# Kernel optimization log

Hardware: AMD Instinct MI355X
Metric: run time of the kernel (lower is better)

## Reference

```python
import jax, jax.numpy as jnp
import numpy as np

N = 100000       # nodes
E = 640000       # edges
G = 2048         # graphs in batch
IN_C, HID, NCLS = 3, 128, 4


def setup_inputs() -> dict:
    key = jax.random.key(0)
    ks = jax.random.split(key, 16)
    x = jax.random.normal(ks[0], (N, IN_C), dtype=jnp.float32)
    edge_index = jax.random.randint(ks[1], (2, E), 0, N, dtype=jnp.int64)
    batch = jnp.sort(jax.random.randint(ks[2], (N,), 0, G, dtype=jnp.int64))
    def glorot(k, shape):
        lim = np.sqrt(6.0 / (shape[0] + shape[1])).astype(np.float32)
        return jax.random.uniform(k, shape, jnp.float32, -lim, lim)
    return {
        "x": x, "edge_index": edge_index, "batch": batch,
        "W1": glorot(ks[3], (IN_C, HID)), "b1": jnp.zeros((HID,), jnp.float32),
        "W2": glorot(ks[4], (HID, HID)),  "b2": jnp.zeros((HID,), jnp.float32),
        "W3": glorot(ks[5], (HID, HID)),  "b3": jnp.zeros((HID,), jnp.float32),
        "W4": glorot(ks[6], (HID, HID)),  "b4": jnp.zeros((HID,), jnp.float32),
        "Wfc": glorot(ks[7], (HID, NCLS)), "bfc": jnp.zeros((NCLS,), jnp.float32),
    }


def _gcn_norm(edge_index):
    # Add self loops, then symmetric normalization D^{-1/2} (A+I) D^{-1/2}.
    loop = jnp.arange(N, dtype=edge_index.dtype)
    row = jnp.concatenate([edge_index[0], loop])  # source
    col = jnp.concatenate([edge_index[1], loop])  # target (aggregation side)
    deg = jax.ops.segment_sum(jnp.ones_like(col, dtype=jnp.float32), col,
                              num_segments=N)
    dinv = jnp.where(deg > 0, jax.lax.rsqrt(deg), 0.0)
    norm = dinv[row] * dinv[col]  # [E+N]
    return row, col, norm


def _gcn_layer(x, W, b, row, col, norm):
    h = x @ W                                 # [N, out]
    msg = h[row] * norm[:, None]              # gather + scale, [E+N, out]
    out = jax.ops.segment_sum(msg, col, num_segments=N)
    return out + b


def reference(x, edge_index, batch, W1, b1, W2, b2, W3, b3, W4, b4, Wfc, bfc):
    row, col, norm = _gcn_norm(edge_index)
    h = jax.nn.relu(_gcn_layer(x, W1, b1, row, col, norm))
    h = jax.nn.relu(_gcn_layer(h, W2, b2, row, col, norm))
    h = jax.nn.relu(_gcn_layer(h, W3, b3, row, col, norm))
    h = jax.nn.relu(_gcn_layer(h, W4, b4, row, col, norm))
    # global mean pool over graphs
    sums = jax.ops.segment_sum(h, batch, num_segments=G)           # [G, HID]
    cnt = jax.ops.segment_sum(jnp.ones((N,), jnp.float32), batch,
                              num_segments=G)
    pooled = sums / jnp.maximum(cnt, 1.0)[:, None]
    return pooled @ Wfc + bfc                                      # [G, NCLS]
```

## Files before the change

kernel.cpp:

```cpp
#include <hip/hip_runtime.h>
#include <hip/hip_bf16.h>

#define N_NODES  100000
#define N_EDGES  640000
#define N_GRAPHS 2048
#define HID      128
#define NB_SCAN  391
#define TILE     32
#define LDW      136

typedef _Float16 half_t;
typedef __attribute__((ext_vector_type(4))) _Float16 half4;
typedef __attribute__((ext_vector_type(8))) _Float16 half8;
typedef __attribute__((ext_vector_type(4))) float floatx4;

__global__ void k_prep(const int* __restrict__ col, int* __restrict__ deg,
                       const float* __restrict__ x, float4* __restrict__ xp,
                       const float* __restrict__ W2, const float* __restrict__ W3,
                       const float* __restrict__ W4, half_t* __restrict__ Wt) {
    int idx = blockIdx.x * 256 + threadIdx.x;
    if (idx < N_EDGES) atomicAdd(&deg[col[idx]], 1);
    if (idx < N_NODES) xp[idx] = make_float4(x[idx * 3 + 0], x[idx * 3 + 1], x[idx * 3 + 2], 0.f);
    if (idx < 3 * 128 * 128) {
        int l = idx >> 14;
        int e = idx & 16383;
        int cin = e >> 7, cout = e & 127;
        const float* W = (l == 0) ? W2 : ((l == 1) ? W3 : W4);
        Wt[l * 16384 + cout * 128 + cin] = (half_t)W[cin * 128 + cout];
    }
}

__global__ void k_scan1(const int* __restrict__ deg, int* __restrict__ row_ptr,
                        int* __restrict__ bsum, float* __restrict__ dinv) {
    __shared__ int s[256];
    int tid = threadIdx.x;
    int i = blockIdx.x * 256 + tid;
    int d = (i < N_NODES) ? deg[i] : 0;
    if (i < N_NODES) dinv[i] = rsqrtf((float)(d + 1));
    s[tid] = d;
    __syncthreads();
    for (int off = 1; off < 256; off <<= 1) {
        int v = (tid >= off) ? s[tid - off] : 0;
        __syncthreads();
        s[tid] += v;
        __syncthreads();
    }
    if (i < N_NODES) row_ptr[i] = s[tid] - d;
    if (tid == 255) bsum[blockIdx.x] = s[255];
}

__global__ void k_scan2(int* __restrict__ bsum) {
    __shared__ int s[512];
    int tid = threadIdx.x;
    int v = (tid < NB_SCAN) ? bsum[tid] : 0;
    s[tid] = v;
    __syncthreads();
    for (int off = 1; off < 512; off <<= 1) {
        int u = (tid >= off) ? s[tid - off] : 0;
        __syncthreads();
        s[tid] += u;
        __syncthreads();
    }
    if (tid < NB_SCAN) bsum[tid] = s[tid] - v;
}

__global__ void k_scan3(int* __restrict__ row_ptr, const int* __restrict__ bsum) {
    int i = blockIdx.x * 256 + threadIdx.x;
    if (i < N_NODES) row_ptr[i] += bsum[blockIdx.x];
    if (i == N_NODES) row_ptr[N_NODES] = N_EDGES;
}

__global__ void k_scatter(const int* __restrict__ row, const int* __restrict__ col,
                          const int* __restrict__ row_ptr, int* __restrict__ cursor,
                          const float* __restrict__ dinv, int2* __restrict__ epair) {
    int e = blockIdx.x * blockDim.x + threadIdx.x;
    if (e >= N_EDGES) return;
    int c = col[e];
    int r = row[e];
    int p = row_ptr[c] + atomicAdd(&cursor[c], 1);
    epair[p] = make_int2(r, __float_as_int(dinv[r] * dinv[c]));
}

__global__ __launch_bounds__(256) void k_aggx_fc1(const float4* __restrict__ xp,
                                                  const int* __restrict__ row_ptr,
                                                  const int2* __restrict__ epair,
                                                  const float* __restrict__ dinv,
                                                  const float* __restrict__ W1,
                                                  const float* __restrict__ b1,
                                                  half_t* __restrict__ h) {
    __shared__ float sax[256][3];
    int t = threadIdx.x;
    int nb = blockIdx.x * 256;
    int i = nb + t;
    if (i < N_NODES) {
        float di = dinv[i];
        float sw = di * di;
        float4 xv = xp[i];
        float a0 = sw * xv.x, a1 = sw * xv.y, a2 = sw * xv.z;
        int s = row_ptr[i], e = row_ptr[i + 1];
        int k = s;
        for (; k + 4 <= e; k += 4) {
            int2 pr[4];
#pragma unroll
            for (int r = 0; r < 4; r++) pr[r] = epair[k + r];
            float4 bx[4];
#pragma unroll
            for (int r = 0; r < 4; r++) bx[r] = xp[pr[r].x];
#pragma unroll
            for (int r = 0; r < 4; r++) {
                float w = __int_as_float(pr[r].y);
                a0 += w * bx[r].x;
                a1 += w * bx[r].y;
                a2 += w * bx[r].z;
            }
        }
        for (; k < e; k++) {
            int2 pr = epair[k];
            float w = __int_as_float(pr.y);
            float4 bx = xp[pr.x];
            a0 += w * bx.x;
            a1 += w * bx.y;
            a2 += w * bx.z;
        }
        sax[t][0] = a0; sax[t][1] = a1; sax[t][2] = a2;
    }
    __syncthreads();
    int cq = t & 31, g8 = t >> 5;
    const float4* W14 = (const float4*)W1;
    float4 w0 = W14[cq], w1 = W14[32 + cq], w2 = W14[64 + cq];
    float4 bb = ((const float4*)b1)[cq];
    for (int pass = 0; pass < 32; pass++) {
        int local = pass * 8 + g8;
        int node = nb + local;
        if (node >= N_NODES) break;
        float x0 = sax[local][0], x1 = sax[local][1], x2 = sax[local][2];
        half4 o;
        o.x = (half_t)fmaxf(bb.x + x0 * w0.x + x1 * w1.x + x2 * w2.x, 0.f);
        o.y = (half_t)fmaxf(bb.y + x0 * w0.y + x1 * w1.y + x2 * w2.y, 0.f);
        o.z = (half_t)fmaxf(bb.z + x0 * w0.z + x1 * w1.z + x2 * w2.z, 0.f);
        o.w = (half_t)fmaxf(bb.w + x0 * w0.w + x1 * w1.w + x2 * w2.w, 0.f);
        ((half4*)h)[(size_t)node * 32 + cq] = o;
    }
}

__global__ __launch_bounds__(256, 8) void k_agg_mm(const half_t* __restrict__ h_in,
                                                   const int* __restrict__ row_ptr,
                                                   const int2* __restrict__ epair,
                                                   const float* __restrict__ dinv,
                                                   const half_t* __restrict__ Wt,
                                                   const float* __restrict__ b,
                                                   half_t* __restrict__ h_out) {
    __shared__ __align__(16) half_t gs[TILE][LDW];
    int tid = threadIdx.x;
    int n0 = blockIdx.x * TILE;
    int lane16 = tid & 15;
    int gidx = tid >> 4;
    const half8* h8 = (const half8*)h_in;

#pragma unroll
    for (int p = 0; p < 2; p++) {
        int local = p * 16 + gidx;
        int i = n0 + local;
        float di = dinv[i];
        float sw = di * di;
        half8 v = h8[(size_t)i * 16 + lane16];
        float acc[8];
#pragma unroll
        for (int c = 0; c < 8; c++) acc[c] = sw * (float)v[c];
        int s = row_ptr[i], e = row_ptr[i + 1];
        if (s < e) {
            int em1 = e - 1;
            int2 p0 = epair[s];
            int k1 = min(s + 1, em1);
            int2 p1 = epair[k1];
            float w0 = __int_as_float(p0.y);
            float w1 = (s + 1 < e) ? __int_as_float(p1.y) : 0.f;
            half8 u0 = h8[(size_t)p0.x * 16 + lane16];
            half8 u1 = h8[(size_t)p1.x * 16 + lane16];
            for (int k = s; k < e; k += 2) {
                int k2 = min(k + 2, em1);
                int k3 = min(k + 3, em1);
                int2 p2 = epair[k2];
                int2 p3 = epair[k3];
                float w2 = (k + 2 < e) ? __int_as_float(p2.y) : 0.f;
                float w3 = (k + 3 < e) ? __int_as_float(p3.y) : 0.f;
                half8 m0 = h8[(size_t)p2.x * 16 + lane16];
                half8 m1 = h8[(size_t)p3.x * 16 + lane16];
#pragma unroll
                for (int c = 0; c < 8; c++) acc[c] += w0 * (float)u0[c] + w1 * (float)u1[c];
                u0 = m0; u1 = m1; w0 = w2; w1 = w3;
            }
        }
        half8 av;
#pragma unroll
        for (int c = 0; c < 8; c++) av[c] = (half_t)acc[c];
        *(half8*)(&gs[local][lane16 * 8]) = av;
    }
    __syncthreads();

    int wv = tid >> 6;
    int ln = tid & 15;
    int q  = (tid >> 4) & 3;
    int rbase = (wv & 1) * 16;
    int cbase = (wv >> 1) * 64;
    floatx4 C[4];
#pragma unroll
    for (int t = 0; t < 4; t++) {
        float bn = b[cbase + t * 16 + ln];
        C[t].x = bn; C[t].y = bn; C[t].z = bn; C[t].w = bn;
    }
#pragma unroll
    for (int kq = 0; kq < 4; kq++) {
        half8 a = *(const half8*)(&gs[rbase + ln][kq * 32 + q * 8]);
#pragma unroll
        for (int t = 0; t < 4; t++) {
            half8 bf = *(const half8*)(Wt + (size_t)(cbase + t * 16 + ln) * 128 + kq * 32 + q * 8);
            C[t] = __builtin_amdgcn_mfma_f32_16x16x32_f16(a, bf, C[t], 0, 0, 0);
        }
    }

    __syncthreads();
#pragma unroll
    for (int t = 0; t < 4; t++) {
#pragma unroll
        for (int reg = 0; reg < 4; reg++) {
            float dv = (reg == 0) ? C[t].x : (reg == 1) ? C[t].y : (reg == 2) ? C[t].z : C[t].w;
            gs[rbase + q * 4 + reg][cbase + t * 16 + ln] = (half_t)fmaxf(dv, 0.f);
        }
    }
    __syncthreads();
#pragma unroll
    for (int v2 = 0; v2 < 2; v2++) {
        int idx = v2 * 256 + tid;
        int r0 = idx >> 4;
        int c0 = idx & 15;
        int4* dst = (int4*)(h_out + (size_t)(n0 + r0) * 128);
        const int4* srcp = (const int4*)(&gs[r0][0]);
        dst[c0] = srcp[c0];
    }
}

__global__ __launch_bounds__(128) void k_pool_final(const half_t* __restrict__ h,
                                                    const int* __restrict__ batch,
                                                    const float* __restrict__ Wfc,
                                                    const float* __restrict__ bfc,
                                                    float* __restrict__ out) {
    __shared__ float sred[8][128];
    __shared__ float red[128][4];
    __shared__ int sb_s, eb_s;
    int g = blockIdx.x, t = threadIdx.x;
    if (t == 0) {
        int lo = 0, hi = N_NODES;
        while (lo < hi) { int mid = (lo + hi) >> 1; if (batch[mid] < g) lo = mid + 1; else hi = mid; }
        sb_s = lo;
        hi = N_NODES;
        while (lo < hi) { int mid = (lo + hi) >> 1; if (batch[mid] < g + 1) lo = mid + 1; else hi = mid; }
        eb_s = lo;
    }
    __syncthreads();
    int sb = sb_s, eb = eb_s;
    int lane16 = t & 15, slot = t >> 4;
    const half8* h8 = (const half8*)h;
    float acc[8];
#pragma unroll
    for (int c = 0; c < 8; c++) acc[c] = 0.f;
    for (int n = sb + slot; n < eb; n += 8) {
        half8 v = h8[(size_t)n * 16 + lane16];
#pragma unroll
        for (int c = 0; c < 8; c++) acc[c] += (float)v[c];
    }
#pragma unroll
    for (int c = 0; c < 8; c++) sred[slot][lane16 * 8 + c] = acc[c];
    __syncthreads();
    float pv = 0.f;
#pragma unroll
    for (int s2 = 0; s2 < 8; s2++) pv += sred[s2][t];
    float inv = 1.0f / fmaxf((float)(eb - sb), 1.0f);
    float v = pv * inv;
    float4 w = ((const float4*)Wfc)[t];
    red[t][0] = v * w.x; red[t][1] = v * w.y; red[t][2] = v * w.z; red[t][3] = v * w.w;
    __syncthreads();
    for (int s = 64; s > 0; s >>= 1) {
        if (t < s) {
            red[t][0] += red[t + s][0];
            red[t][1] += red[t + s][1];
            red[t][2] += red[t + s][2];
            red[t][3] += red[t + s][3];
        }
        __syncthreads();
    }
    if (t < 4) out[g * 4 + t] = red[0][t] + bfc[t];
}

extern "C" void kernel_launch(void* const* d_in, const int* in_sizes, int n_in,
                              void* d_out, int out_size, void* d_ws, size_t ws_size,
                              hipStream_t stream) {
    const float* x     = (const float*)d_in[0];
    const int*   ei    = (const int*)d_in[1];
    const int*   row   = ei;
    const int*   col   = ei + N_EDGES;
    const int*   batch = (const int*)d_in[2];
    const float* W1 = (const float*)d_in[3];
    const float* b1 = (const float*)d_in[4];
    const float* W2 = (const float*)d_in[5];
    const float* b2 = (const float*)d_in[6];
    const float* W3 = (const float*)d_in[7];
    const float* b3 = (const float*)d_in[8];
    const float* W4 = (const float*)d_in[9];
    const float* b4 = (const float*)d_in[10];
    const float* Wfc = (const float*)d_in[11];
    const float* bfc = (const float*)d_in[12];
    float* out = (float*)d_out;

    char* ws = (char*)d_ws;
    size_t off = 0;
    auto take = [&](size_t bytes) -> char* {
        char* p = ws + off;
        off = (off + bytes + 255) & ~(size_t)255;
        return p;
    };
    int*    deg     = (int*)take(N_NODES * 4);
    int*    cursor  = (int*)take(N_NODES * 4);
    size_t  zspan   = (size_t)((char*)cursor + N_NODES * 4 - (char*)deg);
    int*    row_ptr = (int*)take((N_NODES + 1) * 4);
    int*    bsum    = (int*)take(512 * 4);
    float*  dinv    = (float*)take(N_NODES * 4);
    float4* xp      = (float4*)take((size_t)N_NODES * 16);
    int2*   epair   = (int2*)take((size_t)N_EDGES * 8);
    half_t* wt16    = (half_t*)take((size_t)3 * 128 * 128 * 2);
    half_t* bufA    = (half_t*)take((size_t)N_NODES * 128 * 2);
    half_t* bufB    = (half_t*)take((size_t)N_NODES * 128 * 2);

    hipMemsetAsync(deg, 0, zspan, stream);

    k_prep<<<(N_EDGES + 255) / 256, 256, 0, stream>>>(col, deg, x, xp, W2, W3, W4, wt16);
    k_scan1<<<NB_SCAN, 256, 0, stream>>>(deg, row_ptr, bsum, dinv);
    k_scan2<<<1, 512, 0, stream>>>(bsum);
    k_scan3<<<NB_SCAN, 256, 0, stream>>>(row_ptr, bsum);
    k_scatter<<<(N_EDGES + 255) / 256, 256, 0, stream>>>(row, col, row_ptr, cursor,
                                                         dinv, epair);
    k_aggx_fc1<<<NB_SCAN, 256, 0, stream>>>(xp, row_ptr, epair, dinv, W1, b1, bufA);

    const int NBF = N_NODES / TILE;
    k_agg_mm<<<NBF, 256, 0, stream>>>(bufA, row_ptr, epair, dinv, wt16,         b2, bufB);
    k_agg_mm<<<NBF, 256, 0, stream>>>(bufB, row_ptr, epair, dinv, wt16 + 16384, b3, bufA);
    k_agg_mm<<<NBF, 256, 0, stream>>>(bufA, row_ptr, epair, dinv, wt16 + 32768, b4, bufB);

    k_pool_final<<<N_GRAPHS, 128, 0, stream>>>(bufB, batch, Wfc, bfc, out);
}
```

Measured before the change: 318.9 us.

## Halve agg_mm tile to 16 nodes, fuse scan stages, gather fp16 features

The aggregate+matmul kernel now handles 16 nodes per block instead of 32, so each thread aggregates one node and the grid doubles. This raises parallelism for the latency-bound gather but reloads the weight fragments twice as often across blocks. The separate block-sum scan kernel is removed; each scan3 block instead reduces the preceding block sums itself, saving one launch. The first-layer gather reads half-precision packed x, which halves gather bytes at some loss of input precision.

```diff
diff --git a/kernel.cpp b/kernel.cpp
--- a/kernel.cpp
+++ b/kernel.cpp
@@ -6,7 +6,7 @@
 #define N_GRAPHS 2048
 #define HID      128
 #define NB_SCAN  391
-#define TILE     32
+#define TILE     16
 #define LDW      136
 
 typedef _Float16 half_t;
@@ -16,11 +16,18 @@
 
 __global__ void k_prep(const int* __restrict__ col, int* __restrict__ deg,
                        const float* __restrict__ x, float4* __restrict__ xp,
+                       half4* __restrict__ xh,
                        const float* __restrict__ W2, const float* __restrict__ W3,
                        const float* __restrict__ W4, half_t* __restrict__ Wt) {
     int idx = blockIdx.x * 256 + threadIdx.x;
     if (idx < N_EDGES) atomicAdd(&deg[col[idx]], 1);
-    if (idx < N_NODES) xp[idx] = make_float4(x[idx * 3 + 0], x[idx * 3 + 1], x[idx * 3 + 2], 0.f);
+    if (idx < N_NODES) {
+        float x0 = x[idx * 3 + 0], x1 = x[idx * 3 + 1], x2 = x[idx * 3 + 2];
+        xp[idx] = make_float4(x0, x1, x2, 0.f);
+        half4 hv;
+        hv.x = (half_t)x0; hv.y = (half_t)x1; hv.z = (half_t)x2; hv.w = (half_t)0.f;
+        xh[idx] = hv;
+    }
     if (idx < 3 * 128 * 128) {
         int l = idx >> 14;
         int e = idx & 16383;
@@ -49,24 +56,21 @@
     if (tid == 255) bsum[blockIdx.x] = s[255];
 }
 
-__global__ void k_scan2(int* __restrict__ bsum) {
-    __shared__ int s[512];
-    int tid = threadIdx.x;
-    int v = (tid < NB_SCAN) ? bsum[tid] : 0;
-    s[tid] = v;
-    __syncthreads();
-    for (int off = 1; off < 512; off <<= 1) {
-        int u = (tid >= off) ? s[tid - off] : 0;
+__global__ void k_scan3(int* __restrict__ row_ptr, const int* __restrict__ bsum) {
+    __shared__ int sred[256];
+    int t = threadIdx.x, bid = blockIdx.x;
+    int partial = 0;
+    if (t < bid) partial += bsum[t];
+    if (t + 256 < bid) partial += bsum[t + 256];
+    sred[t] = partial;
+    __syncthreads();
+    for (int s = 128; s > 0; s >>= 1) {
+        if (t < s) sred[t] += sred[t + s];
         __syncthreads();
-        s[tid] += u;
-        __syncthreads();
-    }
-    if (tid < NB_SCAN) bsum[tid] = s[tid] - v;
-}
-
-__global__ void k_scan3(int* __restrict__ row_ptr, const int* __restrict__ bsum) {
-    int i = blockIdx.x * 256 + threadIdx.x;
-    if (i < N_NODES) row_ptr[i] += bsum[blockIdx.x];
+    }
+    int add = sred[0];
+    int i = bid * 256 + t;
+    if (i < N_NODES) row_ptr[i] += add;
     if (i == N_NODES) row_ptr[N_NODES] = N_EDGES;
 }
 
@@ -82,6 +86,7 @@
 }
 
 __global__ __launch_bounds__(256) void k_aggx_fc1(const float4* __restrict__ xp,
+                                                  const half4* __restrict__ xh,
                                                   const int* __restrict__ row_ptr,
                                                   const int2* __restrict__ epair,
                                                   const float* __restrict__ dinv,
@@ -103,24 +108,24 @@
             int2 pr[4];
 #pragma unroll
             for (int r = 0; r < 4; r++) pr[r] = epair[k + r];
-            float4 bx[4];
-#pragma unroll
-            for (int r = 0; r < 4; r++) bx[r] = xp[pr[r].x];
+            half4 bx[4];
+#pragma unroll
+            for (int r = 0; r < 4; r++) bx[r] = xh[pr[r].x];
 #pragma unroll
             for (int r = 0; r < 4; r++) {
                 float w = __int_as_float(pr[r].y);
-                a0 += w * bx[r].x;
-                a1 += w * bx[r].y;
-                a2 += w * bx[r].z;
+                a0 += w * (float)bx[r].x;
+                a1 += w * (float)bx[r].y;
+                a2 += w * (float)bx[r].z;
             }
         }
         for (; k < e; k++) {
             int2 pr = epair[k];
             float w = __int_as_float(pr.y);
-            float4 bx = xp[pr.x];
-            a0 += w * bx.x;
-            a1 += w * bx.y;
-            a2 += w * bx.z;
+            half4 bx = xh[pr.x];
+            a0 += w * (float)bx.x;
+            a1 += w * (float)bx.y;
+            a2 += w * (float)bx.z;
         }
         sax[t][0] = a0; sax[t][1] = a1; sax[t][2] = a2;
     }
@@ -157,10 +162,8 @@
     int gidx = tid >> 4;
     const half8* h8 = (const half8*)h_in;
 
-#pragma unroll
-    for (int p = 0; p < 2; p++) {
-        int local = p * 16 + gidx;
-        int i = n0 + local;
+    {
+        int i = n0 + gidx;
         float di = dinv[i];
         float sw = di * di;
         half8 v = h8[(size_t)i * 16 + lane16];
@@ -194,26 +197,25 @@
         half8 av;
 #pragma unroll
         for (int c = 0; c < 8; c++) av[c] = (half_t)acc[c];
-        *(half8*)(&gs[local][lane16 * 8]) = av;
+        *(half8*)(&gs[gidx][lane16 * 8]) = av;
     }
     __syncthreads();
 
     int wv = tid >> 6;
     int ln = tid & 15;
     int q  = (tid >> 4) & 3;
-    int rbase = (wv & 1) * 16;
-    int cbase = (wv >> 1) * 64;
-    floatx4 C[4];
-#pragma unroll
-    for (int t = 0; t < 4; t++) {
+    int cbase = wv * 32;
+    floatx4 C[2];
+#pragma unroll
+    for (int t = 0; t < 2; t++) {
         float bn = b[cbase + t * 16 + ln];
         C[t].x = bn; C[t].y = bn; C[t].z = bn; C[t].w = bn;
     }
 #pragma unroll
     for (int kq = 0; kq < 4; kq++) {
-        half8 a = *(const half8*)(&gs[rbase + ln][kq * 32 + q * 8]);
-#pragma unroll
-        for (int t = 0; t < 4; t++) {
+        half8 a = *(const half8*)(&gs[ln][kq * 32 + q * 8]);
+#pragma unroll
+        for (int t = 0; t < 2; t++) {
             half8 bf = *(const half8*)(Wt + (size_t)(cbase + t * 16 + ln) * 128 + kq * 32 + q * 8);
             C[t] = __builtin_amdgcn_mfma_f32_16x16x32_f16(a, bf, C[t], 0, 0, 0);
         }
@@ -221,19 +223,17 @@
 
     __syncthreads();
 #pragma unroll
-    for (int t = 0; t < 4; t++) {
+    for (int t = 0; t < 2; t++) {
 #pragma unroll
         for (int reg = 0; reg < 4; reg++) {
             float dv = (reg == 0) ? C[t].x : (reg == 1) ? C[t].y : (reg == 2) ? C[t].z : C[t].w;
-            gs[rbase + q * 4 + reg][cbase + t * 16 + ln] = (half_t)fmaxf(dv, 0.f);
-        }
-    }
-    __syncthreads();
-#pragma unroll
-    for (int v2 = 0; v2 < 2; v2++) {
-        int idx = v2 * 256 + tid;
-        int r0 = idx >> 4;
-        int c0 = idx & 15;
+            gs[q * 4 + reg][cbase + t * 16 + ln] = (half_t)fmaxf(dv, 0.f);
+        }
+    }
+    __syncthreads();
+    {
+        int r0 = tid >> 4;
+        int c0 = tid & 15;
         int4* dst = (int4*)(h_out + (size_t)(n0 + r0) * 128);
         const int4* srcp = (const int4*)(&gs[r0][0]);
         dst[c0] = srcp[c0];
@@ -326,6 +326,7 @@
     int*    bsum    = (int*)take(512 * 4);
     float*  dinv    = (float*)take(N_NODES * 4);
     float4* xp      = (float4*)take((size_t)N_NODES * 16);
+    half4*  xh      = (half4*)take((size_t)N_NODES * 8);
     int2*   epair   = (int2*)take((size_t)N_EDGES * 8);
     half_t* wt16    = (half_t*)take((size_t)3 * 128 * 128 * 2);
     half_t* bufA    = (half_t*)take((size_t)N_NODES * 128 * 2);
@@ -333,13 +334,12 @@
 
     hipMemsetAsync(deg, 0, zspan, stream);
 
-    k_prep<<<(N_EDGES + 255) / 256, 256, 0, stream>>>(col, deg, x, xp, W2, W3, W4, wt16);
+    k_prep<<<(N_EDGES + 255) / 256, 256, 0, stream>>>(col, deg, x, xp, xh, W2, W3, W4, wt16);
     k_scan1<<<NB_SCAN, 256, 0, stream>>>(deg, row_ptr, bsum, dinv);
-    k_scan2<<<1, 512, 0, stream>>>(bsum);
     k_scan3<<<NB_SCAN, 256, 0, stream>>>(row_ptr, bsum);
     k_scatter<<<(N_EDGES + 255) / 256, 256, 0, stream>>>(row, col, row_ptr, cursor,
                                                          dinv, epair);
-    k_aggx_fc1<<<NB_SCAN, 256, 0, stream>>>(xp, row_ptr, epair, dinv, W1, b1, bufA);
+    k_aggx_fc1<<<NB_SCAN, 256, 0, stream>>>(xp, xh, row_ptr, epair, dinv, W1, b1, bufA);
 
     const int NBF = N_NODES / TILE;
     k_agg_mm<<<NBF, 256, 0, stream>>>(bufA, row_ptr, epair, dinv, wt16,         b2, bufB);
```

New measurement: 312.8 us. About the same (-1.9%).
